# Optimization experiments

Measured on AMD Instinct MI355X. Metric: run time of the kernel, lower is better.

The kernel has to match this reference:

```python
import jax, jax.numpy as jnp
import numpy as np

EMBED_DIM = 1024
N_HEADS = 16
HEAD_SIZE = EMBED_DIM // N_HEADS
SEQ_LEN = 2048
BATCH = 4


def setup_inputs() -> dict:
    key = jax.random.key(0)
    ks = jax.random.split(key, 9)
    s = 0.02
    d = EMBED_DIM
    return {
        "x": jax.random.normal(ks[0], (BATCH, SEQ_LEN, d), dtype=jnp.float32),
        "wq": jax.random.normal(ks[1], (d, d), dtype=jnp.float32) * s,
        "bq": jnp.zeros((d,), dtype=jnp.float32),
        "wk": jax.random.normal(ks[2], (d, d), dtype=jnp.float32) * s,
        "bk": jnp.zeros((d,), dtype=jnp.float32),
        "wv": jax.random.normal(ks[3], (d, d), dtype=jnp.float32) * s,
        "bv": jnp.zeros((d,), dtype=jnp.float32),
        "wo": jax.random.normal(ks[4], (d, d), dtype=jnp.float32) * s,
        "bo": jnp.zeros((d,), dtype=jnp.float32),
    }


def reference(x, wq, bq, wk, bk, wv, bv, wo, bo):
    b, t, c = x.shape
    h, hs = N_HEADS, HEAD_SIZE
    scale = hs ** -0.5
    # projections (torch Linear: x @ W^T + b); here weights stored as [in, out]
    q = (x @ wq + bq).reshape(b, t, h, hs).transpose(0, 2, 1, 3)  # [b,h,t,hs]
    k = (x @ wk + bk).reshape(b, t, h, hs).transpose(0, 2, 1, 3)
    v = (x @ wv + bv).reshape(b, t, h, hs).transpose(0, 2, 1, 3)
    scores = jnp.einsum('bhqd,bhkd->bhqk', q, k) * scale  # [b,h,t,t]
    causal = jnp.tril(jnp.ones((t, t), dtype=bool))
    scores = jnp.where(causal, scores, -jnp.inf)
    probs = jax.nn.softmax(scores, axis=-1)
    attn = jnp.einsum('bhqk,bhkd->bhqd', probs, v)  # [b,h,t,hs]
    attn = attn.transpose(0, 2, 1, 3).reshape(b, t, c)
    return attn @ wo + bo
```

## Files before the change

### kernel.cpp

```cpp
#include <hip/hip_runtime.h>

#define EMBED 1024
#define NH 16
#define HS 64
#define SEQT 2048
#define NB 4

typedef unsigned short u16;
typedef unsigned int u32;
typedef __attribute__((ext_vector_type(8))) __bf16 bf16x8;
typedef __attribute__((ext_vector_type(4))) float f32x4;
typedef __attribute__((ext_vector_type(4))) unsigned short u16x4;

__device__ __forceinline__ u16 f2bf(float f) {
  __bf16 h = (__bf16)f;
  return __builtin_bit_cast(u16, h);
}

__device__ __forceinline__ void gload_lds16(const void* g, void* l) {
  __builtin_amdgcn_global_load_lds((const __attribute__((address_space(1))) void*)g,
                                   (__attribute__((address_space(3))) void*)l, 16, 0, 0);
}

#define MFMA16(a, b, c) __builtin_amdgcn_mfma_f32_16x16x32_bf16(a, b, c, 0, 0, 0)

__global__ void cvt_x(const float* __restrict__ in, u16* __restrict__ out) {
  int i = (blockIdx.x * 256 + threadIdx.x) * 4;
  float4 v = *(const float4*)(in + i);
  u16x4 o;
  o[0] = f2bf(v.x); o[1] = f2bf(v.y); o[2] = f2bf(v.z); o[3] = f2bf(v.w);
  *(u16x4*)(out + i) = o;
}

__global__ void wtrans(const float* __restrict__ w0, const float* __restrict__ w1,
                       const float* __restrict__ w2, const float* __restrict__ w3,
                       u16* __restrict__ t0, u16* __restrict__ t1,
                       u16* __restrict__ t2, u16* __restrict__ t3) {
  __shared__ float tile[32][33];
  const float* w; u16* t;
  switch (blockIdx.z) {
    case 0: w = w0; t = t0; break;
    case 1: w = w1; t = t1; break;
    case 2: w = w2; t = t2; break;
    default: w = w3; t = t3; break;
  }
  int n0 = blockIdx.x * 32, k0 = blockIdx.y * 32;
  int tx = threadIdx.x, ty = threadIdx.y;
#pragma unroll
  for (int r = 0; r < 4; ++r)
    tile[ty + r * 8][tx] = w[(size_t)(k0 + ty + r * 8) * EMBED + n0 + tx];
  __syncthreads();
#pragma unroll
  for (int r = 0; r < 4; ++r)
    t[(size_t)(n0 + ty + r * 8) * EMBED + k0 + tx] = f2bf(tile[tx][ty + r * 8]);
}

__global__ __launch_bounds__(256, 2) void gemm_qkv(
    const u16* __restrict__ A,
    const u16* __restrict__ wqt, const u16* __restrict__ wkt, const u16* __restrict__ wvt,
    const float* __restrict__ bq, const float* __restrict__ bk, const float* __restrict__ bv,
    u16* __restrict__ qo, u16* __restrict__ ko, u16* __restrict__ vto) {
  __shared__ __align__(16) u16 As[2][4096];
  __shared__ __align__(16) u16 Bs[2][4096];
  int z = blockIdx.z;
  const u16* Bt = (z == 0) ? wqt : ((z == 1) ? wkt : wvt);
  const float* bias = (z == 0) ? bq : ((z == 1) ? bk : bv);
  const float sc = (z == 0) ? 0.18033688011112042f : 1.0f;
  int m0 = blockIdx.y * 128, n0 = blockIdx.x * 128;
  int tid = threadIdx.x, lane = tid & 63, wid = tid >> 6;
  int wr = wid >> 1, wc = wid & 1;
  int lr = lane & 15, lg = lane >> 4;
  int srow = lane >> 2, scol = (lane & 3) * 8;
  f32x4 zero = {0.f, 0.f, 0.f, 0.f};
  f32x4 acc[4][4];
#pragma unroll
  for (int m = 0; m < 4; ++m)
#pragma unroll
    for (int n = 0; n < 4; ++n) acc[m][n] = zero;

  auto STAGE = [&](int k0, int b) {
#pragma unroll
    for (int cc = 0; cc < 2; ++cc) {
      int c = wid * 2 + cc;
      gload_lds16(A + (size_t)(m0 + c * 16 + srow) * EMBED + k0 + scol, &As[b][c * 512]);
      gload_lds16(Bt + (size_t)(n0 + c * 16 + srow) * EMBED + k0 + scol, &Bs[b][c * 512]);
    }
  };

  STAGE(0, 0);
  __syncthreads();
  int cur = 0;
  for (int k0 = 0; k0 < EMBED; k0 += 32) {
    if (k0 + 32 < EMBED) STAGE(k0 + 32, cur ^ 1);
    bf16x8 af[4], bfr[4];
#pragma unroll
    for (int m = 0; m < 4; ++m)
      af[m] = *(const bf16x8*)(&As[cur][(wr * 64 + m * 16 + lr) * 32 + lg * 8]);
#pragma unroll
    for (int n = 0; n < 4; ++n)
      bfr[n] = *(const bf16x8*)(&Bs[cur][(wc * 64 + n * 16 + lr) * 32 + lg * 8]);
    __builtin_amdgcn_s_setprio(1);
#pragma unroll
    for (int m = 0; m < 4; ++m)
#pragma unroll
      for (int n = 0; n < 4; ++n)
        acc[m][n] = MFMA16(af[m], bfr[n], acc[m][n]);
    __builtin_amdgcn_s_setprio(0);
    __syncthreads();
    cur ^= 1;
  }

#pragma unroll
  for (int n = 0; n < 4; ++n) {
    int col = n0 + wc * 64 + n * 16 + lr;
    float bv_ = bias[col];
    int h = col >> 6, d = col & 63;
#pragma unroll
    for (int m = 0; m < 4; ++m) {
      int r0 = m0 + wr * 64 + m * 16 + lg * 4;
      int b_ = r0 >> 11, t_ = r0 & 2047;
      if (z < 2) {
        u16* dst = (z == 0) ? qo : ko;
#pragma unroll
        for (int i = 0; i < 4; ++i)
          dst[(((size_t)(b_ * NH + h)) * SEQT + t_ + i) * HS + d] = f2bf((acc[m][n][i] + bv_) * sc);
      } else {
        u16x4 v;
#pragma unroll
        for (int i = 0; i < 4; ++i) v[i] = f2bf(acc[m][n][i] + bv_);
        *(u16x4*)(vto + (((size_t)(b_ * NH + h)) * HS + d) * SEQT + t_) = v;
      }
    }
  }
}

__global__ __launch_bounds__(256) void flash(
    const u16* __restrict__ q, const u16* __restrict__ k,
    const u16* __restrict__ vt, u16* __restrict__ attnb) {
  __shared__ __align__(16) u16 Ks[2][4096];
  __shared__ __align__(16) u16 Vs[2][4096];
  __shared__ __align__(16) u16 Pl[4][2048];
  const int tid = threadIdx.x, lane = tid & 63, wid = tid >> 6;
  const int lr = lane & 15, lg = lane >> 4;
  const int g = blockIdx.x >> 6, pair = blockIdx.x & 63;
  const u16* Qh = q + (size_t)pair * SEQT * HS;
  const u16* Kh = k + (size_t)pair * SEQT * HS;
  const u16* Vh = vt + (size_t)pair * HS * SEQT;

  const int sr0 = wid * 16 + (lane >> 3);
  const int sc0 = (lane & 7) ^ (sr0 & 7);
  const int sr1 = sr0 + 8;
  const int sc1 = (lane & 7) ^ (sr1 & 7);
  const int koff0 = sr0 * 64 + sc0 * 8;
  const int koff1 = sr1 * 64 + sc1 * 8;
  const size_t voff0 = (size_t)sr0 * SEQT + sc0 * 8;
  const size_t voff1 = (size_t)sr1 * SEQT + sc1 * 8;

  auto STAGE = [&](int t, int b) {
    const u16* Kb = Kh + (size_t)t * 4096;
    const u16* Vb = Vh + (size_t)t * 64;
    gload_lds16(Kb + koff0, &Ks[b][wid * 1024]);
    gload_lds16(Kb + koff1, &Ks[b][wid * 1024 + 512]);
    gload_lds16(Vb + voff0, &Vs[b][wid * 1024]);
    gload_lds16(Vb + voff1, &Vs[b][wid * 1024 + 512]);
  };

  const int b_ = pair >> 4, h = pair & 15;

  for (int ph = 0; ph < 2; ++ph) {
    const int qtile = ph ? (15 - g) : g;
    const int qw = qtile * 128 + wid * 32;

    bf16x8 qf[2][2];
#pragma unroll
    for (int nq = 0; nq < 2; ++nq)
#pragma unroll
      for (int ks = 0; ks < 2; ++ks)
        qf[nq][ks] = *(const bf16x8*)(Qh + (size_t)(qw + nq * 16 + lr) * HS + ks * 32 + lg * 8);

    f32x4 o[2][4];
    const f32x4 zero = {0.f, 0.f, 0.f, 0.f};
#pragma unroll
    for (int mr = 0; mr < 2; ++mr)
#pragma unroll
      for (int nd = 0; nd < 4; ++nd) o[mr][nd] = zero;
    float mrow[2] = {-1e30f, -1e30f}, lrow[2] = {0.f, 0.f};

    const int nt = (qtile + 1) * 2;
    int cur = 0;
    STAGE(0, 0);
    __syncthreads();

    for (int t = 0; t < nt; ++t) {
      if (t + 1 < nt) STAGE(t + 1, cur ^ 1);
      const int k0 = t * 64;

      bf16x8 kf[4][2];
#pragma unroll
      for (int mf = 0; mf < 4; ++mf) {
        const int row = mf * 16 + lr;
#pragma unroll
        for (int ks = 0; ks < 2; ++ks)
          kf[mf][ks] = *(const bf16x8*)(&Ks[cur][row * 64 + ((ks * 4 + lg) ^ (lr & 7)) * 8]);
      }
      f32x4 s[2][4];
      __builtin_amdgcn_s_setprio(1);
#pragma unroll
      for (int nq = 0; nq < 2; ++nq)
#pragma unroll
        for (int mf = 0; mf < 4; ++mf) {
          f32x4 a = zero;
          a = MFMA16(kf[mf][0], qf[nq][0], a);
          a = MFMA16(kf[mf][1], qf[nq][1], a);
          s[nq][mf] = a;
        }
      __builtin_amdgcn_s_setprio(0);
      bf16x8 vf[4][2];
#pragma unroll
      for (int nd = 0; nd < 4; ++nd) {
        const int row = nd * 16 + lr;
#pragma unroll
        for (int ks = 0; ks < 2; ++ks)
          vf[nd][ks] = *(const bf16x8*)(&Vs[cur][row * 64 + ((ks * 4 + lg) ^ (lr & 7)) * 8]);
      }

#pragma unroll
      for (int nq = 0; nq < 2; ++nq) {
        const int qmin = qw + nq * 16;
        if (k0 + 63 > qmin) {
          const int ql = qmin + lr;
#pragma unroll
          for (int mf = 0; mf < 4; ++mf) {
            const int kvb = k0 + mf * 16 + lg * 4;
#pragma unroll
            for (int r = 0; r < 4; ++r)
              if (kvb + r > ql) s[nq][mf][r] = -3.0e38f;
          }
        }
        float t0 = fmaxf(fmaxf(s[nq][0][0], s[nq][0][1]), fmaxf(s[nq][0][2], s[nq][0][3]));
        float t1 = fmaxf(fmaxf(s[nq][1][0], s[nq][1][1]), fmaxf(s[nq][1][2], s[nq][1][3]));
        float t2 = fmaxf(fmaxf(s[nq][2][0], s[nq][2][1]), fmaxf(s[nq][2][2], s[nq][2][3]));
        float t3 = fmaxf(fmaxf(s[nq][3][0], s[nq][3][1]), fmaxf(s[nq][3][2], s[nq][3][3]));
        float mx = fmaxf(fmaxf(t0, t1), fmaxf(t2, t3));
        mx = fmaxf(mx, __shfl_xor(mx, 16, 64));
        mx = fmaxf(mx, __shfl_xor(mx, 32, 64));
        if (__any(mx > mrow[nq] + 8.0f)) {
          const float mn = fmaxf(mrow[nq], mx);
          const float al = exp2f(mrow[nq] - mn);
          mrow[nq] = mn;
          lrow[nq] *= al;
          float ao[4];
#pragma unroll
          for (int r = 0; r < 4; ++r) ao[r] = __shfl(al, lg * 4 + r, 64);
#pragma unroll
          for (int nd = 0; nd < 4; ++nd)
#pragma unroll
            for (int r = 0; r < 4; ++r) o[nq][nd][r] *= ao[r];
        }
        const float mn = mrow[nq];
        float rs = 0.f;
#pragma unroll
        for (int mf = 0; mf < 4; ++mf) {
          u16x4 pk;
#pragma unroll
          for (int r = 0; r < 4; ++r) {
            const float pv = exp2f(s[nq][mf][r] - mn);
            rs += pv;
            pk[r] = f2bf(pv);
          }
          *(u16x4*)(&Pl[wid][(nq * 16 + lr) * 64 +
                             (((2 * mf + (lg >> 1)) ^ (lr & 7)) * 8 + (lg & 1) * 4)]) = pk;
        }
        rs += __shfl_xor(rs, 16, 64);
        rs += __shfl_xor(rs, 32, 64);
        lrow[nq] += rs;
      }

      bf16x8 pa[2][2];
#pragma unroll
      for (int mr = 0; mr < 2; ++mr)
#pragma unroll
        for (int ks = 0; ks < 2; ++ks)
          pa[mr][ks] = *(const bf16x8*)(&Pl[wid][(mr * 16 + lr) * 64 + ((ks * 4 + lg) ^ (lr & 7)) * 8]);
      __builtin_amdgcn_s_setprio(1);
#pragma unroll
      for (int mr = 0; mr < 2; ++mr)
#pragma unroll
        for (int nd = 0; nd < 4; ++nd) {
          o[mr][nd] = MFMA16(pa[mr][0], vf[nd][0], o[mr][nd]);
          o[mr][nd] = MFMA16(pa[mr][1], vf[nd][1], o[mr][nd]);
        }
      __builtin_amdgcn_s_setprio(0);

      __syncthreads();
      cur ^= 1;
    }

#pragma unroll
    for (int mr = 0; mr < 2; ++mr) {
      const float lv = 1.0f / lrow[mr];
      float li[4];
#pragma unroll
      for (int r = 0; r < 4; ++r) li[r] = __shfl(lv, lg * 4 + r, 64);
#pragma unroll
      for (int nd = 0; nd < 4; ++nd) {
        const int d = nd * 16 + lr;
#pragma unroll
        for (int r = 0; r < 4; ++r) {
          const int t_ = qw + mr * 16 + lg * 4 + r;
          attnb[((size_t)(b_ * SEQT + t_)) * EMBED + h * 64 + d] = f2bf(o[mr][nd][r] * li[r]);
        }
      }
    }
  }
}

__global__ __launch_bounds__(256, 2) void gemm_out(
    const u16* __restrict__ A, const u16* __restrict__ wot,
    const float* __restrict__ bo, float* __restrict__ out) {
  __shared__ __align__(16) u16 As[2][4096];
  __shared__ __align__(16) u16 Bs[2][4096];
  int m0 = blockIdx.y * 128, n0 = blockIdx.x * 128;
  int tid = threadIdx.x, lane = tid & 63, wid = tid >> 6;
  int wr = wid >> 1, wc = wid & 1;
  int lr = lane & 15, lg = lane >> 4;
  int srow = lane >> 2, scol = (lane & 3) * 8;
  f32x4 zero = {0.f, 0.f, 0.f, 0.f};
  f32x4 acc[4][4];
#pragma unroll
  for (int m = 0; m < 4; ++m)
#pragma unroll
    for (int n = 0; n < 4; ++n) acc[m][n] = zero;

  auto STAGE = [&](int k0, int b) {
#pragma unroll
    for (int cc = 0; cc < 2; ++cc) {
      int c = wid * 2 + cc;
      gload_lds16(A + (size_t)(m0 + c * 16 + srow) * EMBED + k0 + scol, &As[b][c * 512]);
      gload_lds16(wot + (size_t)(n0 + c * 16 + srow) * EMBED + k0 + scol, &Bs[b][c * 512]);
    }
  };

  STAGE(0, 0);
  __syncthreads();
  int cur = 0;
  for (int k0 = 0; k0 < EMBED; k0 += 32) {
    if (k0 + 32 < EMBED) STAGE(k0 + 32, cur ^ 1);
    bf16x8 af[4], bfr[4];
#pragma unroll
    for (int m = 0; m < 4; ++m)
      af[m] = *(const bf16x8*)(&As[cur][(wr * 64 + m * 16 + lr) * 32 + lg * 8]);
#pragma unroll
    for (int n = 0; n < 4; ++n)
      bfr[n] = *(const bf16x8*)(&Bs[cur][(wc * 64 + n * 16 + lr) * 32 + lg * 8]);
    __builtin_amdgcn_s_setprio(1);
#pragma unroll
    for (int m = 0; m < 4; ++m)
#pragma unroll
      for (int n = 0; n < 4; ++n)
        acc[m][n] = MFMA16(af[m], bfr[n], acc[m][n]);
    __builtin_amdgcn_s_setprio(0);
    __syncthreads();
    cur ^= 1;
  }

#pragma unroll
  for (int n = 0; n < 4; ++n) {
    int col = n0 + wc * 64 + n * 16 + lr;
    float bv_ = bo[col];
#pragma unroll
    for (int m = 0; m < 4; ++m) {
      int r0 = m0 + wr * 64 + m * 16 + lg * 4;
#pragma unroll
      for (int i = 0; i < 4; ++i)
        out[(size_t)(r0 + i) * EMBED + col] = acc[m][n][i] + bv_;
    }
  }
}

extern "C" void kernel_launch(void* const* d_in, const int* in_sizes, int n_in,
                              void* d_out, int out_size, void* d_ws, size_t ws_size,
                              hipStream_t stream) {
  const float* x  = (const float*)d_in[0];
  const float* wq = (const float*)d_in[1];
  const float* bq = (const float*)d_in[2];
  const float* wk = (const float*)d_in[3];
  const float* bk = (const float*)d_in[4];
  const float* wv = (const float*)d_in[5];
  const float* bv = (const float*)d_in[6];
  const float* wo = (const float*)d_in[7];
  const float* bo = (const float*)d_in[8];
  float* out = (float*)d_out;

  char* ws = (char*)d_ws;
  const size_t XB = 16777216;
  const size_t WB = 2097152;
  const size_t QB = 16777216;
  u16* xb    = (u16*)(ws);
  u16* wqbt  = (u16*)(ws + XB);
  u16* wkbt  = (u16*)(ws + XB + WB);
  u16* wvbt  = (u16*)(ws + XB + 2 * WB);
  u16* wobt  = (u16*)(ws + XB + 3 * WB);
  u16* qb    = (u16*)(ws + XB + 4 * WB);
  u16* kb    = (u16*)(ws + XB + 4 * WB + QB);
  u16* vtb   = (u16*)(ws + XB + 4 * WB + 2 * QB);
  u16* attnb = (u16*)(ws + XB + 4 * WB + 3 * QB);

  hipLaunchKernelGGL(cvt_x, dim3(8192), dim3(256), 0, stream, x, xb);
  hipLaunchKernelGGL(wtrans, dim3(32, 32, 4), dim3(32, 8), 0, stream,
                     wq, wk, wv, wo, wqbt, wkbt, wvbt, wobt);
  hipLaunchKernelGGL(gemm_qkv, dim3(8, 64, 3), dim3(256), 0, stream,
                     xb, wqbt, wkbt, wvbt, bq, bk, bv, qb, kb, vtb);
  hipLaunchKernelGGL(flash, dim3(512), dim3(256), 0, stream, qb, kb, vtb, attnb);
  hipLaunchKernelGGL(gemm_out, dim3(8, 64), dim3(256), 0, stream, attnb, wobt, bo, out);
}
```

Before: 295.3 us.

## Deepen GEMM K-tile with swizzled LDS, fuse QKV weights, split flash work per block

Both GEMMs now stage 64-wide K tiles into XOR-swizzled LDS, which halves the number of loop iterations and barriers and is meant to avoid bank conflicts. The QKV GEMM reads one concatenated weight buffer over a 24-wide 2D grid instead of a z-dimension. The flash kernel no longer pairs a short and a long query tile in each block. It launches 1024 blocks, one query tile each, with a launch bound of 3 blocks per CU, trading per-block load balance for more occupancy and scheduler-driven balance. The doubled LDS tiles may reduce GEMM occupancy.

```diff
diff --git a/kernel.cpp b/kernel.cpp
--- a/kernel.cpp
+++ b/kernel.cpp
@@ -56,21 +56,20 @@
 }
 
 __global__ __launch_bounds__(256, 2) void gemm_qkv(
-    const u16* __restrict__ A,
-    const u16* __restrict__ wqt, const u16* __restrict__ wkt, const u16* __restrict__ wvt,
+    const u16* __restrict__ A, const u16* __restrict__ Bt,
     const float* __restrict__ bq, const float* __restrict__ bk, const float* __restrict__ bv,
     u16* __restrict__ qo, u16* __restrict__ ko, u16* __restrict__ vto) {
-  __shared__ __align__(16) u16 As[2][4096];
-  __shared__ __align__(16) u16 Bs[2][4096];
-  int z = blockIdx.z;
-  const u16* Bt = (z == 0) ? wqt : ((z == 1) ? wkt : wvt);
+  __shared__ __align__(16) u16 As[2][8192];
+  __shared__ __align__(16) u16 Bs[2][8192];
+  int m0 = blockIdx.y * 128, n0 = blockIdx.x * 128;
+  int z = n0 >> 10;
   const float* bias = (z == 0) ? bq : ((z == 1) ? bk : bv);
   const float sc = (z == 0) ? 0.18033688011112042f : 1.0f;
-  int m0 = blockIdx.y * 128, n0 = blockIdx.x * 128;
   int tid = threadIdx.x, lane = tid & 63, wid = tid >> 6;
   int wr = wid >> 1, wc = wid & 1;
   int lr = lane & 15, lg = lane >> 4;
-  int srow = lane >> 2, scol = (lane & 3) * 8;
+  const int srow_in = lane >> 3;
+  const int scol_sw = ((lane & 7) ^ (lane >> 3)) * 8;
   f32x4 zero = {0.f, 0.f, 0.f, 0.f};
   f32x4 acc[4][4];
 #pragma unroll
@@ -80,31 +79,39 @@
 
   auto STAGE = [&](int k0, int b) {
 #pragma unroll
-    for (int cc = 0; cc < 2; ++cc) {
-      int c = wid * 2 + cc;
-      gload_lds16(A + (size_t)(m0 + c * 16 + srow) * EMBED + k0 + scol, &As[b][c * 512]);
-      gload_lds16(Bt + (size_t)(n0 + c * 16 + srow) * EMBED + k0 + scol, &Bs[b][c * 512]);
+    for (int j = 0; j < 4; ++j) {
+      int rb = (j * 4 + wid) * 8;
+      gload_lds16(A + (size_t)(m0 + rb + srow_in) * EMBED + k0 + scol_sw, &As[b][rb * 64]);
+      gload_lds16(Bt + (size_t)(n0 + rb + srow_in) * EMBED + k0 + scol_sw, &Bs[b][rb * 64]);
     }
   };
 
   STAGE(0, 0);
   __syncthreads();
   int cur = 0;
-  for (int k0 = 0; k0 < EMBED; k0 += 32) {
-    if (k0 + 32 < EMBED) STAGE(k0 + 32, cur ^ 1);
-    bf16x8 af[4], bfr[4];
+  for (int k0 = 0; k0 < EMBED; k0 += 64) {
+    if (k0 + 64 < EMBED) STAGE(k0 + 64, cur ^ 1);
+    bf16x8 af[4][2], bfr[4][2];
 #pragma unroll
     for (int m = 0; m < 4; ++m)
-      af[m] = *(const bf16x8*)(&As[cur][(wr * 64 + m * 16 + lr) * 32 + lg * 8]);
+#pragma unroll
+      for (int kk = 0; kk < 2; ++kk)
+        af[m][kk] = *(const bf16x8*)(&As[cur][(wr * 64 + m * 16 + lr) * 64 +
+                                              (((kk * 4 + lg) ^ (lr & 7)) * 8)]);
 #pragma unroll
     for (int n = 0; n < 4; ++n)
-      bfr[n] = *(const bf16x8*)(&Bs[cur][(wc * 64 + n * 16 + lr) * 32 + lg * 8]);
+#pragma unroll
+      for (int kk = 0; kk < 2; ++kk)
+        bfr[n][kk] = *(const bf16x8*)(&Bs[cur][(wc * 64 + n * 16 + lr) * 64 +
+                                               (((kk * 4 + lg) ^ (lr & 7)) * 8)]);
     __builtin_amdgcn_s_setprio(1);
 #pragma unroll
     for (int m = 0; m < 4; ++m)
 #pragma unroll
-      for (int n = 0; n < 4; ++n)
-        acc[m][n] = MFMA16(af[m], bfr[n], acc[m][n]);
+      for (int n = 0; n < 4; ++n) {
+        acc[m][n] = MFMA16(af[m][0], bfr[n][0], acc[m][n]);
+        acc[m][n] = MFMA16(af[m][1], bfr[n][1], acc[m][n]);
+      }
     __builtin_amdgcn_s_setprio(0);
     __syncthreads();
     cur ^= 1;
@@ -113,8 +120,9 @@
 #pragma unroll
   for (int n = 0; n < 4; ++n) {
     int col = n0 + wc * 64 + n * 16 + lr;
-    float bv_ = bias[col];
-    int h = col >> 6, d = col & 63;
+    int lcol = col & 1023;
+    float bv_ = bias[lcol];
+    int h = lcol >> 6, d = lcol & 63;
 #pragma unroll
     for (int m = 0; m < 4; ++m) {
       int r0 = m0 + wr * 64 + m * 16 + lg * 4;
@@ -134,7 +142,7 @@
   }
 }
 
-__global__ __launch_bounds__(256) void flash(
+__global__ __launch_bounds__(256, 3) void flash(
     const u16* __restrict__ q, const u16* __restrict__ k,
     const u16* __restrict__ vt, u16* __restrict__ attnb) {
   __shared__ __align__(16) u16 Ks[2][4096];
@@ -143,6 +151,7 @@
   const int tid = threadIdx.x, lane = tid & 63, wid = tid >> 6;
   const int lr = lane & 15, lg = lane >> 4;
   const int g = blockIdx.x >> 6, pair = blockIdx.x & 63;
+  const int qtile = 15 - g;
   const u16* Qh = q + (size_t)pair * SEQT * HS;
   const u16* Kh = k + (size_t)pair * SEQT * HS;
   const u16* Vh = vt + (size_t)pair * HS * SEQT;
@@ -166,150 +175,146 @@
   };
 
   const int b_ = pair >> 4, h = pair & 15;
-
-  for (int ph = 0; ph < 2; ++ph) {
-    const int qtile = ph ? (15 - g) : g;
-    const int qw = qtile * 128 + wid * 32;
-
-    bf16x8 qf[2][2];
+  const int qw = qtile * 128 + wid * 32;
+
+  bf16x8 qf[2][2];
+#pragma unroll
+  for (int nq = 0; nq < 2; ++nq)
+#pragma unroll
+    for (int ks = 0; ks < 2; ++ks)
+      qf[nq][ks] = *(const bf16x8*)(Qh + (size_t)(qw + nq * 16 + lr) * HS + ks * 32 + lg * 8);
+
+  f32x4 o[2][4];
+  const f32x4 zero = {0.f, 0.f, 0.f, 0.f};
+#pragma unroll
+  for (int mr = 0; mr < 2; ++mr)
+#pragma unroll
+    for (int nd = 0; nd < 4; ++nd) o[mr][nd] = zero;
+  float mrow[2] = {-1e30f, -1e30f}, lrow[2] = {0.f, 0.f};
+
+  const int nt = (qtile + 1) * 2;
+  int cur = 0;
+  STAGE(0, 0);
+  __syncthreads();
+
+  for (int t = 0; t < nt; ++t) {
+    if (t + 1 < nt) STAGE(t + 1, cur ^ 1);
+    const int k0 = t * 64;
+
+    bf16x8 kf[4][2];
+#pragma unroll
+    for (int mf = 0; mf < 4; ++mf) {
+      const int row = mf * 16 + lr;
+#pragma unroll
+      for (int ks = 0; ks < 2; ++ks)
+        kf[mf][ks] = *(const bf16x8*)(&Ks[cur][row * 64 + ((ks * 4 + lg) ^ (lr & 7)) * 8]);
+    }
+    f32x4 s[2][4];
+    __builtin_amdgcn_s_setprio(1);
 #pragma unroll
     for (int nq = 0; nq < 2; ++nq)
 #pragma unroll
+      for (int mf = 0; mf < 4; ++mf) {
+        f32x4 a = zero;
+        a = MFMA16(kf[mf][0], qf[nq][0], a);
+        a = MFMA16(kf[mf][1], qf[nq][1], a);
+        s[nq][mf] = a;
+      }
+    __builtin_amdgcn_s_setprio(0);
+    bf16x8 vf[4][2];
+#pragma unroll
+    for (int nd = 0; nd < 4; ++nd) {
+      const int row = nd * 16 + lr;
+#pragma unroll
       for (int ks = 0; ks < 2; ++ks)
-        qf[nq][ks] = *(const bf16x8*)(Qh + (size_t)(qw + nq * 16 + lr) * HS + ks * 32 + lg * 8);
-
-    f32x4 o[2][4];
-    const f32x4 zero = {0.f, 0.f, 0.f, 0.f};
+        vf[nd][ks] = *(const bf16x8*)(&Vs[cur][row * 64 + ((ks * 4 + lg) ^ (lr & 7)) * 8]);
+    }
+
+#pragma unroll
+    for (int nq = 0; nq < 2; ++nq) {
+      const int qmin = qw + nq * 16;
+      if (k0 + 63 > qmin) {
+        const int ql = qmin + lr;
+#pragma unroll
+        for (int mf = 0; mf < 4; ++mf) {
+          const int kvb = k0 + mf * 16 + lg * 4;
+#pragma unroll
+          for (int r = 0; r < 4; ++r)
+            if (kvb + r > ql) s[nq][mf][r] = -3.0e38f;
+        }
+      }
+      float t0 = fmaxf(fmaxf(s[nq][0][0], s[nq][0][1]), fmaxf(s[nq][0][2], s[nq][0][3]));
+      float t1 = fmaxf(fmaxf(s[nq][1][0], s[nq][1][1]), fmaxf(s[nq][1][2], s[nq][1][3]));
+      float t2 = fmaxf(fmaxf(s[nq][2][0], s[nq][2][1]), fmaxf(s[nq][2][2], s[nq][2][3]));
+      float t3 = fmaxf(fmaxf(s[nq][3][0], s[nq][3][1]), fmaxf(s[nq][3][2], s[nq][3][3]));
+      float mx = fmaxf(fmaxf(t0, t1), fmaxf(t2, t3));
+      mx = fmaxf(mx, __shfl_xor(mx, 16, 64));
+      mx = fmaxf(mx, __shfl_xor(mx, 32, 64));
+      if (__any(mx > mrow[nq] + 8.0f)) {
+        const float mn = fmaxf(mrow[nq], mx);
+        const float al = exp2f(mrow[nq] - mn);
+        mrow[nq] = mn;
+        lrow[nq] *= al;
+        float ao[4];
+#pragma unroll
+        for (int r = 0; r < 4; ++r) ao[r] = __shfl(al, lg * 4 + r, 64);
+#pragma unroll
+        for (int nd = 0; nd < 4; ++nd)
+#pragma unroll
+          for (int r = 0; r < 4; ++r) o[nq][nd][r] *= ao[r];
+      }
+      const float mn = mrow[nq];
+      float rs = 0.f;
+#pragma unroll
+      for (int mf = 0; mf < 4; ++mf) {
+        u16x4 pk;
+#pragma unroll
+        for (int r = 0; r < 4; ++r) {
+          const float pv = exp2f(s[nq][mf][r] - mn);
+          rs += pv;
+          pk[r] = f2bf(pv);
+        }
+        *(u16x4*)(&Pl[wid][(nq * 16 + lr) * 64 +
+                           (((2 * mf + (lg >> 1)) ^ (lr & 7)) * 8 + (lg & 1) * 4)]) = pk;
+      }
+      rs += __shfl_xor(rs, 16, 64);
+      rs += __shfl_xor(rs, 32, 64);
+      lrow[nq] += rs;
+    }
+
+    bf16x8 pa[2][2];
 #pragma unroll
     for (int mr = 0; mr < 2; ++mr)
 #pragma unroll
-      for (int nd = 0; nd < 4; ++nd) o[mr][nd] = zero;
-    float mrow[2] = {-1e30f, -1e30f}, lrow[2] = {0.f, 0.f};
-
-    const int nt = (qtile + 1) * 2;
-    int cur = 0;
-    STAGE(0, 0);
+      for (int ks = 0; ks < 2; ++ks)
+        pa[mr][ks] = *(const bf16x8*)(&Pl[wid][(mr * 16 + lr) * 64 + ((ks * 4 + lg) ^ (lr & 7)) * 8]);
+    __builtin_amdgcn_s_setprio(1);
+#pragma unroll
+    for (int mr = 0; mr < 2; ++mr)
+#pragma unroll
+      for (int nd = 0; nd < 4; ++nd) {
+        o[mr][nd] = MFMA16(pa[mr][0], vf[nd][0], o[mr][nd]);
+        o[mr][nd] = MFMA16(pa[mr][1], vf[nd][1], o[mr][nd]);
+      }
+    __builtin_amdgcn_s_setprio(0);
+
     __syncthreads();
-
-    for (int t = 0; t < nt; ++t) {
-      if (t + 1 < nt) STAGE(t + 1, cur ^ 1);
-      const int k0 = t * 64;
-
-      bf16x8 kf[4][2];
-#pragma unroll
-      for (int mf = 0; mf < 4; ++mf) {
-        const int row = mf * 16 + lr;
-#pragma unroll
-        for (int ks = 0; ks < 2; ++ks)
-          kf[mf][ks] = *(const bf16x8*)(&Ks[cur][row * 64 + ((ks * 4 + lg) ^ (lr & 7)) * 8]);
-      }
-      f32x4 s[2][4];
-      __builtin_amdgcn_s_setprio(1);
-#pragma unroll
-      for (int nq = 0; nq < 2; ++nq)
-#pragma unroll
-        for (int mf = 0; mf < 4; ++mf) {
-          f32x4 a = zero;
-          a = MFMA16(kf[mf][0], qf[nq][0], a);
-          a = MFMA16(kf[mf][1], qf[nq][1], a);
-          s[nq][mf] = a;
-        }
-      __builtin_amdgcn_s_setprio(0);
-      bf16x8 vf[4][2];
-#pragma unroll
-      for (int nd = 0; nd < 4; ++nd) {
-        const int row = nd * 16 + lr;
-#pragma unroll
-        for (int ks = 0; ks < 2; ++ks)
-          vf[nd][ks] = *(const bf16x8*)(&Vs[cur][row * 64 + ((ks * 4 + lg) ^ (lr & 7)) * 8]);
-      }
-
-#pragma unroll
-      for (int nq = 0; nq < 2; ++nq) {
-        const int qmin = qw + nq * 16;
-        if (k0 + 63 > qmin) {
-          const int ql = qmin + lr;
-#pragma unroll
-          for (int mf = 0; mf < 4; ++mf) {
-            const int kvb = k0 + mf * 16 + lg * 4;
-#pragma unroll
-            for (int r = 0; r < 4; ++r)
-              if (kvb + r > ql) s[nq][mf][r] = -3.0e38f;
-          }
-        }
-        float t0 = fmaxf(fmaxf(s[nq][0][0], s[nq][0][1]), fmaxf(s[nq][0][2], s[nq][0][3]));
-        float t1 = fmaxf(fmaxf(s[nq][1][0], s[nq][1][1]), fmaxf(s[nq][1][2], s[nq][1][3]));
-        float t2 = fmaxf(fmaxf(s[nq][2][0], s[nq][2][1]), fmaxf(s[nq][2][2], s[nq][2][3]));
-        float t3 = fmaxf(fmaxf(s[nq][3][0], s[nq][3][1]), fmaxf(s[nq][3][2], s[nq][3][3]));
-        float mx = fmaxf(fmaxf(t0, t1), fmaxf(t2, t3));
-        mx = fmaxf(mx, __shfl_xor(mx, 16, 64));
-        mx = fmaxf(mx, __shfl_xor(mx, 32, 64));
-        if (__any(mx > mrow[nq] + 8.0f)) {
-          const float mn = fmaxf(mrow[nq], mx);
-          const float al = exp2f(mrow[nq] - mn);
-          mrow[nq] = mn;
-          lrow[nq] *= al;
-          float ao[4];
-#pragma unroll
-          for (int r = 0; r < 4; ++r) ao[r] = __shfl(al, lg * 4 + r, 64);
-#pragma unroll
-          for (int nd = 0; nd < 4; ++nd)
-#pragma unroll
-            for (int r = 0; r < 4; ++r) o[nq][nd][r] *= ao[r];
-        }
-        const float mn = mrow[nq];
-        float rs = 0.f;
-#pragma unroll
-        for (int mf = 0; mf < 4; ++mf) {
-          u16x4 pk;
-#pragma unroll
-          for (int r = 0; r < 4; ++r) {
-            const float pv = exp2f(s[nq][mf][r] - mn);
-            rs += pv;
-            pk[r] = f2bf(pv);
-          }
-          *(u16x4*)(&Pl[wid][(nq * 16 + lr) * 64 +
-                             (((2 * mf + (lg >> 1)) ^ (lr & 7)) * 8 + (lg & 1) * 4)]) = pk;
-        }
-        rs += __shfl_xor(rs, 16, 64);
-        rs += __shfl_xor(rs, 32, 64);
-        lrow[nq] += rs;
-      }
-
-      bf16x8 pa[2][2];
-#pragma unroll
-      for (int mr = 0; mr < 2; ++mr)
-#pragma unroll
-        for (int ks = 0; ks < 2; ++ks)
-          pa[mr][ks] = *(const bf16x8*)(&Pl[wid][(mr * 16 + lr) * 64 + ((ks * 4 + lg) ^ (lr & 7)) * 8]);
-      __builtin_amdgcn_s_setprio(1);
-#pragma unroll
-      for (int mr = 0; mr < 2; ++mr)
-#pragma unroll
-        for (int nd = 0; nd < 4; ++nd) {
-          o[mr][nd] = MFMA16(pa[mr][0], vf[nd][0], o[mr][nd]);
-          o[mr][nd] = MFMA16(pa[mr][1], vf[nd][1], o[mr][nd]);
-        }
-      __builtin_amdgcn_s_setprio(0);
-
-      __syncthreads();
-      cur ^= 1;
-    }
-
-#pragma unroll
-    for (int mr = 0; mr < 2; ++mr) {
-      const float lv = 1.0f / lrow[mr];
-      float li[4];
-#pragma unroll
-      for (int r = 0; r < 4; ++r) li[r] = __shfl(lv, lg * 4 + r, 64);
-#pragma unroll
-      for (int nd = 0; nd < 4; ++nd) {
-        const int d = nd * 16 + lr;
-#pragma unroll
-        for (int r = 0; r < 4; ++r) {
-          const int t_ = qw + mr * 16 + lg * 4 + r;
-          attnb[((size_t)(b_ * SEQT + t_)) * EMBED + h * 64 + d] = f2bf(o[mr][nd][r] * li[r]);
-        }
+    cur ^= 1;
+  }
+
+#pragma unroll
+  for (int mr = 0; mr < 2; ++mr) {
+    const float lv = 1.0f / lrow[mr];
+    float li[4];
+#pragma unroll
+    for (int r = 0; r < 4; ++r) li[r] = __shfl(lv, lg * 4 + r, 64);
+#pragma unroll
+    for (int nd = 0; nd < 4; ++nd) {
+      const int d = nd * 16 + lr;
+#pragma unroll
+      for (int r = 0; r < 4; ++r) {
+        const int t_ = qw + mr * 16 + lg * 4 + r;
+        attnb[((size_t)(b_ * SEQT + t_)) * EMBED + h * 64 + d] = f2bf(o[mr][nd][r] * li[r]);
       }
     }
   }
@@ -318,13 +323,14 @@
 __global__ __launch_bounds__(256, 2) void gemm_out(
     const u16* __restrict__ A, const u16* __restrict__ wot,
     const float* __restrict__ bo, float* __restrict__ out) {
-  __shared__ __align__(16) u16 As[2][4096];
-  __shared__ __align__(16) u16 Bs[2][4096];
+  __shared__ __align__(16) u16 As[2][8192];
+  __shared__ __align__(16) u16 Bs[2][8192];
   int m0 = blockIdx.y * 128, n0 = blockIdx.x * 128;
   int tid = threadIdx.x, lane = tid & 63, wid = tid >> 6;
   int wr = wid >> 1, wc = wid & 1;
   int lr = lane & 15, lg = lane >> 4;
-  int srow = lane >> 2, scol = (lane & 3) * 8;
+  const int srow_in = lane >> 3;
+  const int scol_sw = ((lane & 7) ^ (lane >> 3)) * 8;
   f32x4 zero = {0.f, 0.f, 0.f, 0.f};
   f32x4 acc[4][4];
 #pragma unroll
@@ -334,31 +340,39 @@
 
   auto STAGE = [&](int k0, int b) {
 #pragma unroll
-    for (int cc = 0; cc < 2; ++cc) {
-      int c = wid * 2 + cc;
-      gload_lds16(A + (size_t)(m0 + c * 16 + srow) * EMBED + k0 + scol, &As[b][c * 512]);
-      gload_lds16(wot + (size_t)(n0 + c * 16 + srow) * EMBED + k0 + scol, &Bs[b][c * 512]);
+    for (int j = 0; j < 4; ++j) {
+      int rb = (j * 4 + wid) * 8;
+      gload_lds16(A + (size_t)(m0 + rb + srow_in) * EMBED + k0 + scol_sw, &As[b][rb * 64]);
+      gload_lds16(wot + (size_t)(n0 + rb + srow_in) * EMBED + k0 + scol_sw, &Bs[b][rb * 64]);
     }
   };
 
   STAGE(0, 0);
   __syncthreads();
   int cur = 0;
-  for (int k0 = 0; k0 < EMBED; k0 += 32) {
-    if (k0 + 32 < EMBED) STAGE(k0 + 32, cur ^ 1);
-    bf16x8 af[4], bfr[4];
+  for (int k0 = 0; k0 < EMBED; k0 += 64) {
+    if (k0 + 64 < EMBED) STAGE(k0 + 64, cur ^ 1);
+    bf16x8 af[4][2], bfr[4][2];
 #pragma unroll
     for (int m = 0; m < 4; ++m)
-      af[m] = *(const bf16x8*)(&As[cur][(wr * 64 + m * 16 + lr) * 32 + lg * 8]);
+#pragma unroll
+      for (int kk = 0; kk < 2; ++kk)
+        af[m][kk] = *(const bf16x8*)(&As[cur][(wr * 64 + m * 16 + lr) * 64 +
+                                              (((kk * 4 + lg) ^ (lr & 7)) * 8)]);
 #pragma unroll
     for (int n = 0; n < 4; ++n)
-      bfr[n] = *(const bf16x8*)(&Bs[cur][(wc * 64 + n * 16 + lr) * 32 + lg * 8]);
+#pragma unroll
+      for (int kk = 0; kk < 2; ++kk)
+        bfr[n][kk] = *(const bf16x8*)(&Bs[cur][(wc * 64 + n * 16 + lr) * 64 +
+                                               (((kk * 4 + lg) ^ (lr & 7)) * 8)]);
     __builtin_amdgcn_s_setprio(1);
 #pragma unroll
     for (int m = 0; m < 4; ++m)
 #pragma unroll
-      for (int n = 0; n < 4; ++n)
-        acc[m][n] = MFMA16(af[m], bfr[n], acc[m][n]);
+      for (int n = 0; n < 4; ++n) {
+        acc[m][n] = MFMA16(af[m][0], bfr[n][0], acc[m][n]);
+        acc[m][n] = MFMA16(af[m][1], bfr[n][1], acc[m][n]);
+      }
     __builtin_amdgcn_s_setprio(0);
     __syncthreads();
     cur ^= 1;
@@ -396,21 +410,20 @@
   const size_t XB = 16777216;
   const size_t WB = 2097152;
   const size_t QB = 16777216;
-  u16* xb    = (u16*)(ws);
-  u16* wqbt  = (u16*)(ws + XB);
-  u16* wkbt  = (u16*)(ws + XB + WB);
-  u16* wvbt  = (u16*)(ws + XB + 2 * WB);
-  u16* wobt  = (u16*)(ws + XB + 3 * WB);
-  u16* qb    = (u16*)(ws + XB + 4 * WB);
-  u16* kb    = (u16*)(ws + XB + 4 * WB + QB);
-  u16* vtb   = (u16*)(ws + XB + 4 * WB + 2 * QB);
-  u16* attnb = (u16*)(ws + XB + 4 * WB + 3 * QB);
+  u16* xb     = (u16*)(ws);
+  u16* wqkvbt = (u16*)(ws + XB);
+  u16* wobt   = (u16*)(ws + XB + 3 * WB);
+  u16* qb     = (u16*)(ws + XB + 4 * WB);
+  u16* kb     = (u16*)(ws + XB + 4 * WB + QB);
+  u16* vtb    = (u16*)(ws + XB + 4 * WB + 2 * QB);
+  u16* attnb  = (u16*)(ws + XB + 4 * WB + 3 * QB);
 
   hipLaunchKernelGGL(cvt_x, dim3(8192), dim3(256), 0, stream, x, xb);
   hipLaunchKernelGGL(wtrans, dim3(32, 32, 4), dim3(32, 8), 0, stream,
-                     wq, wk, wv, wo, wqbt, wkbt, wvbt, wobt);
-  hipLaunchKernelGGL(gemm_qkv, dim3(8, 64, 3), dim3(256), 0, stream,
-                     xb, wqbt, wkbt, wvbt, bq, bk, bv, qb, kb, vtb);
-  hipLaunchKernelGGL(flash, dim3(512), dim3(256), 0, stream, qb, kb, vtb, attnb);
+                     wq, wk, wv, wo,
+                     wqkvbt, wqkvbt + 1048576, wqkvbt + 2097152, wobt);
+  hipLaunchKernelGGL(gemm_qkv, dim3(24, 64), dim3(256), 0, stream,
+                     xb, wqkvbt, bq, bk, bv, qb, kb, vtb);
+  hipLaunchKernelGGL(flash, dim3(1024), dim3(256), 0, stream, qb, kb, vtb, attnb);
   hipLaunchKernelGGL(gemm_out, dim3(8, 64), dim3(256), 0, stream, attnb, wobt, bo, out);
 }
```

Result: faster. 262.9 us (-11.0%).
